# Performance work log

Hardware: AMD Instinct MI355X
Metric: run time of the kernel (lower is better)

Reference implementation:

```python
import jax, jax.numpy as jnp
import numpy as np

L = 104          # atom feature / hidden dim (self.length)
NUM_CLASSES = 500
D, N, P = 256, 1024, 8  # DAGs, nodes per DAG (topo-ordered), max predecessors


def setup_inputs() -> dict:
    key = jax.random.key(0)
    ks = jax.random.split(key, 8)
    atom_features = jax.random.normal(ks[0], (D, N, L), dtype=jnp.float32)

    # Padded predecessor lists; pred_idx[d, n, p] < n guarantees topological order 0..N-1.
    rng = np.random.default_rng(0)
    base = np.floor(rng.random((D, N, P)) * np.maximum(np.arange(N), 1)[None, :, None]).astype(np.int32)
    keep = rng.random((D, N, P)) < 0.6
    keep[:, :, 0] = True                      # every non-root node has >=1 predecessor
    pred_idx = np.where(keep, base, -1)
    pred_idx[:, 0, :] = -1                    # node 0 is the root (no predecessors)
    pred_idx = jnp.asarray(pred_idx, dtype=jnp.int32)

    s1 = float(1.0 / np.sqrt(L))
    s2 = float(1.0 / np.sqrt(2 * L))
    W_single = jax.random.uniform(ks[1], (L, L), minval=-s1, maxval=s1)
    b_single = jax.random.uniform(ks[2], (L,), minval=-s1, maxval=s1)
    W_merge = jax.random.uniform(ks[3], (L, 2 * L), minval=-s2, maxval=s2)
    b_merge = jax.random.uniform(ks[4], (L,), minval=-s2, maxval=s2)
    attn_w = jax.random.uniform(ks[5], (L,))   # torch.rand(length)
    dag_w = jax.random.uniform(ks[6], (L,))
    W_final = jax.random.uniform(ks[7], (NUM_CLASSES, L), minval=-s1, maxval=s1)
    b_final = jnp.zeros((NUM_CLASSES,), jnp.float32)
    return {
        "atom_features": atom_features, "pred_idx": pred_idx,
        "W_single": W_single, "b_single": b_single,
        "W_merge": W_merge, "b_merge": b_merge,
        "attn_w": attn_w, "dag_w": dag_w,
        "W_final": W_final, "b_final": b_final,
    }


def _forward(atom_features, pred_idx, W_single, b_single, W_merge, b_merge,
             attn_w, dag_w, W_final, b_final):
    n_nodes = atom_features.shape[1]

    def per_dag(feats, preds):  # feats [N, L], preds [N, P]
        def step(outputs, n):
            feat = feats[n]                                   # [L]
            p = preds[n]                                      # [P]
            valid = p >= 0                                    # [P]
            po = outputs[jnp.clip(p, 0, n_nodes - 1)]         # [P, L] gathered predecessor outputs
            # softmax over the predecessor (stacking) dim, weighted by attention_weight
            logits = jnp.where(valid[:, None], attn_w * po, -1e30)
            agg = jnp.sum(jax.nn.softmax(logits, axis=0) * po * valid[:, None].astype(po.dtype), axis=0)  # [L]
            merged = jax.nn.relu(W_merge @ jnp.concatenate([agg, feat]) + b_merge)
            root = jax.nn.relu(W_single @ feat + b_single)
            out = jnp.where(jnp.any(valid), merged, root)     # [L]
            return outputs.at[n].set(out), None
        outputs, _ = jax.lax.scan(step, jnp.zeros_like(feats), jnp.arange(n_nodes))
        return outputs[-1]                                    # output of last (sink) node

    last = jax.vmap(per_dag)(atom_features, pred_idx)         # [D, L]
    w = jax.nn.softmax(dag_w * last, axis=0)                  # softmax over DAG dim
    pooled = jnp.sum(w * last, axis=0)                        # [L]
    return pooled @ W_final.T + b_final                       # [NUM_CLASSES]


def reference(atom_features, pred_idx, W_single, b_single, W_merge, b_merge,
              attn_w, dag_w, W_final, b_final):
    return _forward(atom_features, pred_idx, W_single, b_single, W_merge, b_merge,
                    attn_w, dag_w, W_final, b_final)
```

## Files before the change

kernel.cpp:

```cpp
#include <hip/hip_runtime.h>

#define DN  256
#define NN  1024
#define PP  8
#define LL  104
#define CLS 500
#define BT  512
#define TMAX 64
#define KP  232
#define NG  26

typedef __attribute__((ext_vector_type(8))) short short8;
typedef __attribute__((ext_vector_type(4))) short short4v;
typedef __attribute__((ext_vector_type(4))) float f32x4;

#define MFMA(a, b, c) __builtin_amdgcn_mfma_f32_16x16x32_bf16((a), (b), (c), 0, 0, 0)

__device__ __forceinline__ void split_bf16(float x, unsigned short& h, unsigned short& l) {
    unsigned u = __float_as_uint(x);
    h = (unsigned short)(u >> 16);
    float hf = __uint_as_float(u & 0xFFFF0000u);
    l = (unsigned short)(__float_as_uint(x - hf) >> 16);
}

__global__ __launch_bounds__(BT, 2) void dag_level_kernel(
    const float* __restrict__ atom,
    const int*   __restrict__ pred,
    const float* __restrict__ W_single,
    const float* __restrict__ b_single,
    const float* __restrict__ W_merge,
    const float* __restrict__ b_merge,
    const float* __restrict__ attn_w,
    float* __restrict__ out_all,
    float* __restrict__ last_buf)
{
    __shared__ __align__(16) unsigned short x_hi[TMAX][KP];
    __shared__ __align__(16) unsigned short x_lo[TMAX][KP];
    __shared__ int   lvl[NN];
    __shared__ int   cnt[NN];
    __shared__ unsigned short order[NN];
    __shared__ __align__(16) float s_attn2[LL];
    __shared__ float s_bm[LL];
    __shared__ int   csum[64];
    __shared__ int   s_flag, s_maxlvl;

    const int d    = blockIdx.x;
    const int tid  = threadIdx.x;
    const int wid  = tid >> 6;
    const int lane = tid & 63;
    const int p    = wid & 3;

    const float* atom_d = atom + (size_t)d * NN * LL;
    const int*   pred_d = pred + (size_t)d * NN * PP;
    float*       out_d  = out_all + (size_t)d * NN * LL;

    short8 wh[2][7], wl[2][7];
    #pragma unroll
    for (int h = 0; h < 2; ++h) {
        const int r = (2*p + h)*16 + (lane & 15);
        #pragma unroll
        for (int kt = 0; kt < 7; ++kt) {
            const int k0 = kt*32 + (lane >> 4)*8;
            short8 hh, lo8;
            #pragma unroll
            for (int j = 0; j < 8; ++j) {
                float v = (r < LL && (k0 + j) < 2*LL) ? W_merge[r*2*LL + k0 + j] : 0.f;
                unsigned short a, b;
                split_bf16(v, a, b);
                hh[j] = (short)a; lo8[j] = (short)b;
            }
            wh[h][kt] = hh; wl[h][kt] = lo8;
        }
    }

    for (int idx = tid; idx < TMAX * (KP - 2*LL); idx += BT) {
        int rr = idx / (KP - 2*LL), cc = 2*LL + (idx - rr*(KP - 2*LL));
        x_hi[rr][cc] = 0; x_lo[rr][cc] = 0;
    }
    if (tid < LL) { s_attn2[tid] = attn_w[tid] * 1.44269504f; s_bm[tid] = b_merge[tid]; }
    if (tid == 0) { s_flag = 0; s_maxlvl = 0; }

    {
        int mypA[PP], mypB[PP];
        const int4* p4 = (const int4*)(pred_d + tid * PP);
        int4 a = p4[0], b = p4[1];
        mypA[0]=a.x; mypA[1]=a.y; mypA[2]=a.z; mypA[3]=a.w;
        mypA[4]=b.x; mypA[5]=b.y; mypA[6]=b.z; mypA[7]=b.w;
        const int4* q4 = (const int4*)(pred_d + (tid + BT) * PP);
        int4 c = q4[0], e = q4[1];
        mypB[0]=c.x; mypB[1]=c.y; mypB[2]=c.z; mypB[3]=c.w;
        mypB[4]=e.x; mypB[5]=e.y; mypB[6]=e.z; mypB[7]=e.w;
        lvl[tid] = 0; lvl[tid + BT] = 0;
        __syncthreads();
        for (int it = 1; it <= NN; ++it) {
            int mxA = -1, mxB = -1;
            #pragma unroll
            for (int q = 0; q < PP; ++q) {
                if (mypA[q] >= 0) mxA = max(mxA, lvl[mypA[q]]);
                if (mypB[q] >= 0) mxB = max(mxB, lvl[mypB[q]]);
            }
            bool ch = false;
            if (mxA + 1 != lvl[tid])      { lvl[tid]      = mxA + 1; ch = true; }
            if (mxB + 1 != lvl[tid + BT]) { lvl[tid + BT] = mxB + 1; ch = true; }
            if (ch) s_flag = it;
            __syncthreads();
            int f = s_flag;
            __syncthreads();
            if (f != it) break;
        }
        atomicMax(&s_maxlvl, max(lvl[tid], lvl[tid + BT]));
    }

    cnt[tid] = 0; cnt[tid + BT] = 0;
    __syncthreads();
    atomicAdd(&cnt[lvl[tid]], 1);
    atomicAdd(&cnt[lvl[tid + BT]], 1);
    __syncthreads();
    if (tid < 64) { int s = 0; for (int i = 0; i < 16; ++i) s += cnt[tid*16 + i]; csum[tid] = s; }
    __syncthreads();
    if (tid == 0) { int run = 0; for (int t = 0; t < 64; ++t) { int c = csum[t]; csum[t] = run; run += c; } }
    __syncthreads();
    if (tid < 64) {
        int run = csum[tid];
        for (int i = 0; i < 16; ++i) { int c = cnt[tid*16 + i]; cnt[tid*16 + i] = run; run += c; }
    }
    __syncthreads();
    {
        int pos = atomicAdd(&cnt[lvl[tid]], 1);      order[pos] = (unsigned short)tid;
        pos     = atomicAdd(&cnt[lvl[tid + BT]], 1); order[pos] = (unsigned short)(tid + BT);
    }
    __syncthreads();

    {
        int nroots = cnt[0];
        for (int task = tid; task < nroots * LL; task += BT) {
            int ni = task / LL, r = task - ni * LL;
            int n = order[ni];
            float acc = b_single[r];
            const float* feat = atom_d + n * LL;
            const float* wr = W_single + r * LL;
            #pragma unroll 8
            for (int l = 0; l < LL; ++l) acc = fmaf(wr[l], feat[l], acc);
            float v = fmaxf(acc, 0.f);
            out_d[n * LL + r] = v;
            if (n == NN - 1) last_buf[d * LL + r] = v;
        }
    }
    __syncthreads();

    const int maxlvl = s_maxlvl;
    for (int L = 1; L <= maxlvl; ++L) {
        const int s = cnt[L - 1], e = cnt[L];
        for (int t0 = s; t0 < e; t0 += TMAX) {
            const int tc = min(TMAX, e - t0);

            const int ntask = tc * NG;
            for (int task = tid; task < ntask; task += BT) {
                int ni = task / NG;
                int lg = task - ni * NG;
                int n  = order[t0 + ni];
                const int4* pp4 = (const int4*)(pred_d + n * PP);
                int4 pa = pp4[0], pb = pp4[1];
                int pi[PP] = {pa.x, pa.y, pa.z, pa.w, pb.x, pb.y, pb.z, pb.w};
                float4 po4[PP];
                #pragma unroll
                for (int q = 0; q < PP; ++q) {
                    int idx = max(pi[q], 0);
                    po4[q] = *(const float4*)&out_d[idx * LL + lg * 4];
                }
                float4 ft = *(const float4*)&atom_d[n * LL + lg * 4];
                float4 aw = *(const float4*)&s_attn2[lg * 4];
                float po[PP][4];
                #pragma unroll
                for (int q = 0; q < PP; ++q) {
                    po[q][0] = po4[q].x; po[q][1] = po4[q].y;
                    po[q][2] = po4[q].z; po[q][3] = po4[q].w;
                }
                float awv[4] = {aw.x, aw.y, aw.z, aw.w};
                float ftv[4] = {ft.x, ft.y, ft.z, ft.w};
                unsigned short oh[8], ol[8];
                #pragma unroll
                for (int f = 0; f < 4; ++f) {
                    float den = 0.f, num = 0.f;
                    #pragma unroll
                    for (int q = 0; q < PP; ++q) {
                        float e2 = exp2f(awv[f] * po[q][f]);
                        e2 = (pi[q] >= 0) ? e2 : 0.f;
                        den += e2;
                        num = fmaf(e2, po[q][f], num);
                    }
                    float agg = __fdividef(num, den);
                    split_bf16(agg,    oh[f],     ol[f]);
                    split_bf16(ftv[f], oh[4 + f], ol[4 + f]);
                }
                short4v h0 = {(short)oh[0], (short)oh[1], (short)oh[2], (short)oh[3]};
                short4v l0 = {(short)ol[0], (short)ol[1], (short)ol[2], (short)ol[3]};
                short4v h1 = {(short)oh[4], (short)oh[5], (short)oh[6], (short)oh[7]};
                short4v l1 = {(short)ol[4], (short)ol[5], (short)ol[6], (short)ol[7]};
                *(short4v*)&x_hi[ni][lg*4]      = h0;
                *(short4v*)&x_lo[ni][lg*4]      = l0;
                *(short4v*)&x_hi[ni][LL + lg*4] = h1;
                *(short4v*)&x_lo[ni][LL + lg*4] = l1;
            }
            __syncthreads();

            const int mts = (tc + 15) >> 4;
            const int njobs = mts * 4;
            for (int job = wid; job < njobs; job += 8) {
                const int mt = job >> 2;
                const int row_a = mt*16 + (lane & 15);
                const int kg = (lane >> 4) * 8;
                f32x4 a0 = {0.f,0.f,0.f,0.f}, b0 = {0.f,0.f,0.f,0.f}, c0 = {0.f,0.f,0.f,0.f};
                f32x4 a1 = {0.f,0.f,0.f,0.f}, b1 = {0.f,0.f,0.f,0.f}, c1 = {0.f,0.f,0.f,0.f};
                #pragma unroll
                for (int kt = 0; kt < 7; ++kt) {
                    const int k0 = kt*32 + kg;
                    short8 ah = *(const short8*)&x_hi[row_a][k0];
                    short8 al = *(const short8*)&x_lo[row_a][k0];
                    a0 = MFMA(ah, wh[0][kt], a0);
                    b0 = MFMA(ah, wl[0][kt], b0);
                    c0 = MFMA(al, wh[0][kt], c0);
                    if (p < 3) {
                        a1 = MFMA(ah, wh[1][kt], a1);
                        b1 = MFMA(ah, wl[1][kt], b1);
                        c1 = MFMA(al, wh[1][kt], c1);
                    }
                }
                f32x4 acc0 = a0 + b0 + c0;
                f32x4 acc1 = a1 + b1 + c1;
                const int r0 = p*32 + (lane & 15);
                #pragma unroll
                for (int j = 0; j < 4; ++j) {
                    int ni = mt*16 + (lane >> 4)*4 + j;
                    if (ni < tc) {
                        int n = order[t0 + ni];
                        if (r0 < LL) {
                            float v = fmaxf(acc0[j] + s_bm[r0], 0.f);
                            out_d[n*LL + r0] = v;
                            if (n == NN - 1) last_buf[d*LL + r0] = v;
                        }
                        if (p < 3) {
                            const int r1 = r0 + 16;
                            float v = fmaxf(acc1[j] + s_bm[r1], 0.f);
                            out_d[n*LL + r1] = v;
                            if (n == NN - 1) last_buf[d*LL + r1] = v;
                        }
                    }
                }
            }
            __syncthreads();
        }
    }
}

__global__ __launch_bounds__(256) void final_pool_kernel(
    const float* __restrict__ last_buf,
    const float* __restrict__ dag_w,
    const float* __restrict__ W_final,
    const float* __restrict__ b_final,
    float* __restrict__ out)
{
    __shared__ float s_pooled[LL];
    const int tid = threadIdx.x;

    if (tid < LL) {
        float dw = dag_w[tid];
        float m = -1e30f;
        #pragma unroll 8
        for (int dd = 0; dd < DN; ++dd)
            m = fmaxf(m, dw * last_buf[dd * LL + tid]);
        float den = 0.f, num = 0.f;
        #pragma unroll 8
        for (int dd = 0; dd < DN; ++dd) {
            float v = last_buf[dd * LL + tid];
            float e = __expf(dw * v - m);
            den += e;
            num = fmaf(e, v, num);
        }
        s_pooled[tid] = num / den;
    }
    __syncthreads();

    for (int c = tid; c < CLS; c += 256) {
        float acc = b_final[c];
        const float* wr = W_final + c * LL;
        #pragma unroll 8
        for (int l = 0; l < LL; ++l) acc = fmaf(wr[l], s_pooled[l], acc);
        out[c] = acc;
    }
}

extern "C" void kernel_launch(void* const* d_in, const int* in_sizes, int n_in,
                              void* d_out, int out_size, void* d_ws, size_t ws_size,
                              hipStream_t stream) {
    const float* atom     = (const float*)d_in[0];
    const int*   pred     = (const int*)  d_in[1];
    const float* W_single = (const float*)d_in[2];
    const float* b_single = (const float*)d_in[3];
    const float* W_merge  = (const float*)d_in[4];
    const float* b_merge  = (const float*)d_in[5];
    const float* attn_w   = (const float*)d_in[6];
    const float* dag_w    = (const float*)d_in[7];
    const float* W_final  = (const float*)d_in[8];
    const float* b_final  = (const float*)d_in[9];
    float* out = (float*)d_out;

    float* out_all  = (float*)d_ws;
    float* last_buf = out_all + (size_t)DN * NN * LL;

    dag_level_kernel<<<DN, BT, 0, stream>>>(atom, pred, W_single, b_single,
                                            W_merge, b_merge, attn_w,
                                            out_all, last_buf);
    final_pool_kernel<<<1, 256, 0, stream>>>(last_buf, dag_w, W_final, b_final, out);
}
```

Measured before the change: 367.5 us.

## Software-pipeline predecessor gathers and assign one output tile per wave

The aggregation loop is software-pipelined with two register stages, so the global gathers for the next task are issued before the softmax math of the current one, hiding memory latency. The MFMA stage changes from four waves each holding two 16-row weight tiles to seven waves each holding one tile and looping over all node tiles. This halves the per-wave weight registers and spreads the matmul over more waves, but it leaves one wave idle and doubles the live gather registers. The duplicated loads clamp the task index to stay in range.

```diff
diff --git a/kernel.cpp b/kernel.cpp
--- a/kernel.cpp
+++ b/kernel.cpp
@@ -48,16 +48,14 @@
     const int tid  = threadIdx.x;
     const int wid  = tid >> 6;
     const int lane = tid & 63;
-    const int p    = wid & 3;
 
     const float* atom_d = atom + (size_t)d * NN * LL;
     const int*   pred_d = pred + (size_t)d * NN * PP;
     float*       out_d  = out_all + (size_t)d * NN * LL;
 
-    short8 wh[2][7], wl[2][7];
-    #pragma unroll
-    for (int h = 0; h < 2; ++h) {
-        const int r = (2*p + h)*16 + (lane & 15);
+    short8 wh[7], wl[7];
+    {
+        const int r = min(wid, 6)*16 + (lane & 15);
         #pragma unroll
         for (int kt = 0; kt < 7; ++kt) {
             const int k0 = kt*32 + (lane >> 4)*8;
@@ -69,7 +67,7 @@
                 split_bf16(v, a, b);
                 hh[j] = (short)a; lo8[j] = (short)b;
             }
-            wh[h][kt] = hh; wl[h][kt] = lo8;
+            wh[kt] = hh; wl[kt] = lo8;
         }
     }
 
@@ -148,102 +146,102 @@
     }
     __syncthreads();
 
+#define DECLP(S) int pi##S[PP]; float4 po##S[PP]; float4 ft##S; int ni##S, lg##S;
+
+#define LOADP(S, TASK)                                                          \
+    {                                                                           \
+        int tt_ = min((TASK), ntask - 1);                                       \
+        ni##S = tt_ / NG; lg##S = tt_ - ni##S * NG;                             \
+        int n_ = order[t0 + ni##S];                                             \
+        const int4* pp4_ = (const int4*)(pred_d + n_ * PP);                     \
+        int4 pa_ = pp4_[0], pb_ = pp4_[1];                                      \
+        pi##S[0]=pa_.x; pi##S[1]=pa_.y; pi##S[2]=pa_.z; pi##S[3]=pa_.w;         \
+        pi##S[4]=pb_.x; pi##S[5]=pb_.y; pi##S[6]=pb_.z; pi##S[7]=pb_.w;         \
+        ft##S = *(const float4*)&atom_d[n_ * LL + lg##S * 4];                   \
+        _Pragma("unroll")                                                       \
+        for (int q_ = 0; q_ < PP; ++q_) {                                       \
+            int idx_ = max(pi##S[q_], 0);                                       \
+            po##S[q_] = *(const float4*)&out_d[idx_ * LL + lg##S * 4];          \
+        }                                                                       \
+    }
+
+#define COMPP(S)                                                                \
+    {                                                                           \
+        float4 aw_ = *(const float4*)&s_attn2[lg##S * 4];                       \
+        float awv_[4] = {aw_.x, aw_.y, aw_.z, aw_.w};                           \
+        float ftv_[4] = {ft##S.x, ft##S.y, ft##S.z, ft##S.w};                   \
+        unsigned short oh_[8], ol_[8];                                          \
+        _Pragma("unroll")                                                       \
+        for (int f_ = 0; f_ < 4; ++f_) {                                        \
+            float den_ = 0.f, num_ = 0.f;                                       \
+            _Pragma("unroll")                                                   \
+            for (int q_ = 0; q_ < PP; ++q_) {                                   \
+                float pv_ = ((const float*)&po##S[q_])[f_];                     \
+                float e_ = exp2f(awv_[f_] * pv_);                               \
+                e_ = (pi##S[q_] >= 0) ? e_ : 0.f;                               \
+                den_ += e_;                                                     \
+                num_ = fmaf(e_, pv_, num_);                                     \
+            }                                                                   \
+            float agg_ = __fdividef(num_, den_);                                \
+            split_bf16(agg_,      oh_[f_],     ol_[f_]);                        \
+            split_bf16(ftv_[f_],  oh_[4+f_],   ol_[4+f_]);                      \
+        }                                                                       \
+        short4v h0_ = {(short)oh_[0], (short)oh_[1], (short)oh_[2], (short)oh_[3]}; \
+        short4v l0_ = {(short)ol_[0], (short)ol_[1], (short)ol_[2], (short)ol_[3]}; \
+        short4v h1_ = {(short)oh_[4], (short)oh_[5], (short)oh_[6], (short)oh_[7]}; \
+        short4v l1_ = {(short)ol_[4], (short)ol_[5], (short)ol_[6], (short)ol_[7]}; \
+        *(short4v*)&x_hi[ni##S][lg##S*4]      = h0_;                            \
+        *(short4v*)&x_lo[ni##S][lg##S*4]      = l0_;                            \
+        *(short4v*)&x_hi[ni##S][LL + lg##S*4] = h1_;                            \
+        *(short4v*)&x_lo[ni##S][LL + lg##S*4] = l1_;                            \
+    }
+
     const int maxlvl = s_maxlvl;
     for (int L = 1; L <= maxlvl; ++L) {
         const int s = cnt[L - 1], e = cnt[L];
         for (int t0 = s; t0 < e; t0 += TMAX) {
             const int tc = min(TMAX, e - t0);
-
             const int ntask = tc * NG;
-            for (int task = tid; task < ntask; task += BT) {
-                int ni = task / NG;
-                int lg = task - ni * NG;
-                int n  = order[t0 + ni];
-                const int4* pp4 = (const int4*)(pred_d + n * PP);
-                int4 pa = pp4[0], pb = pp4[1];
-                int pi[PP] = {pa.x, pa.y, pa.z, pa.w, pb.x, pb.y, pb.z, pb.w};
-                float4 po4[PP];
-                #pragma unroll
-                for (int q = 0; q < PP; ++q) {
-                    int idx = max(pi[q], 0);
-                    po4[q] = *(const float4*)&out_d[idx * LL + lg * 4];
+
+            {
+                DECLP(A) DECLP(B)
+                LOADP(A, tid)
+                for (int t = tid; t < ntask; t += 2*BT) {
+                    LOADP(B, t + BT)
+                    COMPP(A)
+                    if (t + 2*BT < ntask) LOADP(A, t + 2*BT)
+                    COMPP(B)
                 }
-                float4 ft = *(const float4*)&atom_d[n * LL + lg * 4];
-                float4 aw = *(const float4*)&s_attn2[lg * 4];
-                float po[PP][4];
-                #pragma unroll
-                for (int q = 0; q < PP; ++q) {
-                    po[q][0] = po4[q].x; po[q][1] = po4[q].y;
-                    po[q][2] = po4[q].z; po[q][3] = po4[q].w;
-                }
-                float awv[4] = {aw.x, aw.y, aw.z, aw.w};
-                float ftv[4] = {ft.x, ft.y, ft.z, ft.w};
-                unsigned short oh[8], ol[8];
-                #pragma unroll
-                for (int f = 0; f < 4; ++f) {
-                    float den = 0.f, num = 0.f;
-                    #pragma unroll
-                    for (int q = 0; q < PP; ++q) {
-                        float e2 = exp2f(awv[f] * po[q][f]);
-                        e2 = (pi[q] >= 0) ? e2 : 0.f;
-                        den += e2;
-                        num = fmaf(e2, po[q][f], num);
-                    }
-                    float agg = __fdividef(num, den);
-                    split_bf16(agg,    oh[f],     ol[f]);
-                    split_bf16(ftv[f], oh[4 + f], ol[4 + f]);
-                }
-                short4v h0 = {(short)oh[0], (short)oh[1], (short)oh[2], (short)oh[3]};
-                short4v l0 = {(short)ol[0], (short)ol[1], (short)ol[2], (short)ol[3]};
-                short4v h1 = {(short)oh[4], (short)oh[5], (short)oh[6], (short)oh[7]};
-                short4v l1 = {(short)ol[4], (short)ol[5], (short)ol[6], (short)ol[7]};
-                *(short4v*)&x_hi[ni][lg*4]      = h0;
-                *(short4v*)&x_lo[ni][lg*4]      = l0;
-                *(short4v*)&x_hi[ni][LL + lg*4] = h1;
-                *(short4v*)&x_lo[ni][LL + lg*4] = l1;
             }
             __syncthreads();
 
-            const int mts = (tc + 15) >> 4;
-            const int njobs = mts * 4;
-            for (int job = wid; job < njobs; job += 8) {
-                const int mt = job >> 2;
-                const int row_a = mt*16 + (lane & 15);
+            if (wid < 7) {
+                const int mts = (tc + 15) >> 4;
                 const int kg = (lane >> 4) * 8;
-                f32x4 a0 = {0.f,0.f,0.f,0.f}, b0 = {0.f,0.f,0.f,0.f}, c0 = {0.f,0.f,0.f,0.f};
-                f32x4 a1 = {0.f,0.f,0.f,0.f}, b1 = {0.f,0.f,0.f,0.f}, c1 = {0.f,0.f,0.f,0.f};
-                #pragma unroll
-                for (int kt = 0; kt < 7; ++kt) {
-                    const int k0 = kt*32 + kg;
-                    short8 ah = *(const short8*)&x_hi[row_a][k0];
-                    short8 al = *(const short8*)&x_lo[row_a][k0];
-                    a0 = MFMA(ah, wh[0][kt], a0);
-                    b0 = MFMA(ah, wl[0][kt], b0);
-                    c0 = MFMA(al, wh[0][kt], c0);
-                    if (p < 3) {
-                        a1 = MFMA(ah, wh[1][kt], a1);
-                        b1 = MFMA(ah, wl[1][kt], b1);
-                        c1 = MFMA(al, wh[1][kt], c1);
+                const int r0 = wid*16 + (lane & 15);
+                for (int mt = 0; mt < mts; ++mt) {
+                    const int row_a = mt*16 + (lane & 15);
+                    f32x4 a0 = {0.f,0.f,0.f,0.f}, b0 = {0.f,0.f,0.f,0.f}, c0 = {0.f,0.f,0.f,0.f};
+                    #pragma unroll
+                    for (int kt = 0; kt < 7; ++kt) {
+                        const int k0 = kt*32 + kg;
+                        short8 ah = *(const short8*)&x_hi[row_a][k0];
+                        short8 al = *(const short8*)&x_lo[row_a][k0];
+                        a0 = MFMA(ah, wh[kt], a0);
+                        b0 = MFMA(ah, wl[kt], b0);
+                        c0 = MFMA(al, wh[kt], c0);
                     }
-                }
-                f32x4 acc0 = a0 + b0 + c0;
-                f32x4 acc1 = a1 + b1 + c1;
-                const int r0 = p*32 + (lane & 15);
-                #pragma unroll
-                for (int j = 0; j < 4; ++j) {
-                    int ni = mt*16 + (lane >> 4)*4 + j;
-                    if (ni < tc) {
-                        int n = order[t0 + ni];
-                        if (r0 < LL) {
-                            float v = fmaxf(acc0[j] + s_bm[r0], 0.f);
-                            out_d[n*LL + r0] = v;
-                            if (n == NN - 1) last_buf[d*LL + r0] = v;
-                        }
-                        if (p < 3) {
-                            const int r1 = r0 + 16;
-                            float v = fmaxf(acc1[j] + s_bm[r1], 0.f);
-                            out_d[n*LL + r1] = v;
-                            if (n == NN - 1) last_buf[d*LL + r1] = v;
+                    f32x4 acc = a0 + b0 + c0;
+                    if (r0 < LL) {
+                        #pragma unroll
+                        for (int j = 0; j < 4; ++j) {
+                            int ni = mt*16 + (lane >> 4)*4 + j;
+                            if (ni < tc) {
+                                int n = order[t0 + ni];
+                                float v = fmaxf(acc[j] + s_bm[r0], 0.f);
+                                out_d[n*LL + r0] = v;
+                                if (n == NN - 1) last_buf[d*LL + r0] = v;
+                            }
                         }
                     }
                 }
@@ -251,6 +249,9 @@
             __syncthreads();
         }
     }
+#undef DECLP
+#undef LOADP
+#undef COMPP
 }
 
 __global__ __launch_bounds__(256) void final_pool_kernel(
```

After: 401.1 us. 1.09x slower.

## Prefetch next level's gathers during MFMA and stage predecessor lists in LDS

Applied to the files above, without the earlier changes.

Copies the predecessor index table into LDS once and uses it for level computation and gathers. Before the merge GEMM of the current tile, it issues the next tile's feature loads and predecessor-output loads, reloading only predecessors that sit at the level being computed now. It also doubles the relaxation steps per barrier in level assignment and remaps the MFMA work so seven waves each own one 16-row slice of the weights. The aim is to hide global-memory latency behind the MFMA phase and reduce barriers, at the cost of more registers and 32KB more LDS, which may reduce occupancy.

```diff
diff --git a/kernel.cpp b/kernel.cpp
--- a/kernel.cpp
+++ b/kernel.cpp
@@ -21,6 +21,39 @@
     h = (unsigned short)(u >> 16);
     float hf = __uint_as_float(u & 0xFFFF0000u);
     l = (unsigned short)(__float_as_uint(x - hf) >> 16);
+}
+
+__device__ __forceinline__ void sm_store(int ni, int lg, const int pi[PP],
+    const float4 pv[PP], float4 ft, const float* s_attn2,
+    unsigned short (*xh)[KP], unsigned short (*xl)[KP])
+{
+    float4 aw = *(const float4*)&s_attn2[lg * 4];
+    float awv[4] = {aw.x, aw.y, aw.z, aw.w};
+    float ftv[4] = {ft.x, ft.y, ft.z, ft.w};
+    unsigned short oh[8], ol[8];
+    #pragma unroll
+    for (int f = 0; f < 4; ++f) {
+        float den = 0.f, num = 0.f;
+        #pragma unroll
+        for (int q = 0; q < PP; ++q) {
+            float pvq = ((const float*)&pv[q])[f];
+            float e2 = exp2f(awv[f] * pvq);
+            e2 = (pi[q] >= 0) ? e2 : 0.f;
+            den += e2;
+            num = fmaf(e2, pvq, num);
+        }
+        float agg = __fdividef(num, den);
+        split_bf16(agg,    oh[f],     ol[f]);
+        split_bf16(ftv[f], oh[4 + f], ol[4 + f]);
+    }
+    short4v h0 = {(short)oh[0], (short)oh[1], (short)oh[2], (short)oh[3]};
+    short4v l0 = {(short)ol[0], (short)ol[1], (short)ol[2], (short)ol[3]};
+    short4v h1 = {(short)oh[4], (short)oh[5], (short)oh[6], (short)oh[7]};
+    short4v l1 = {(short)ol[4], (short)ol[5], (short)ol[6], (short)ol[7]};
+    *(short4v*)&xh[ni][lg*4]      = h0;
+    *(short4v*)&xl[ni][lg*4]      = l0;
+    *(short4v*)&xh[ni][LL + lg*4] = h1;
+    *(short4v*)&xl[ni][LL + lg*4] = l1;
 }
 
 __global__ __launch_bounds__(BT, 2) void dag_level_kernel(
@@ -36,6 +69,7 @@
 {
     __shared__ __align__(16) unsigned short x_hi[TMAX][KP];
     __shared__ __align__(16) unsigned short x_lo[TMAX][KP];
+    __shared__ __align__(16) int pred_lds[NN][PP];
     __shared__ int   lvl[NN];
     __shared__ int   cnt[NN];
     __shared__ unsigned short order[NN];
@@ -48,16 +82,17 @@
     const int tid  = threadIdx.x;
     const int wid  = tid >> 6;
     const int lane = tid & 63;
-    const int p    = wid & 3;
 
     const float* atom_d = atom + (size_t)d * NN * LL;
     const int*   pred_d = pred + (size_t)d * NN * PP;
     float*       out_d  = out_all + (size_t)d * NN * LL;
 
-    short8 wh[2][7], wl[2][7];
-    #pragma unroll
-    for (int h = 0; h < 2; ++h) {
-        const int r = (2*p + h)*16 + (lane & 15);
+    for (int idx = tid; idx < NN * PP / 4; idx += BT)
+        ((int4*)pred_lds)[idx] = ((const int4*)pred_d)[idx];
+
+    short8 wh[7], wl[7];
+    {
+        const int r = min(wid, 6)*16 + (lane & 15);
         #pragma unroll
         for (int kt = 0; kt < 7; ++kt) {
             const int k0 = kt*32 + (lane >> 4)*8;
@@ -69,7 +104,7 @@
                 split_bf16(v, a, b);
                 hh[j] = (short)a; lo8[j] = (short)b;
             }
-            wh[h][kt] = hh; wl[h][kt] = lo8;
+            wh[kt] = hh; wl[kt] = lo8;
         }
     }
 
@@ -79,29 +114,26 @@
     }
     if (tid < LL) { s_attn2[tid] = attn_w[tid] * 1.44269504f; s_bm[tid] = b_merge[tid]; }
     if (tid == 0) { s_flag = 0; s_maxlvl = 0; }
+    lvl[tid] = 0; lvl[tid + BT] = 0;
+    __syncthreads();
 
     {
         int mypA[PP], mypB[PP];
-        const int4* p4 = (const int4*)(pred_d + tid * PP);
-        int4 a = p4[0], b = p4[1];
-        mypA[0]=a.x; mypA[1]=a.y; mypA[2]=a.z; mypA[3]=a.w;
-        mypA[4]=b.x; mypA[5]=b.y; mypA[6]=b.z; mypA[7]=b.w;
-        const int4* q4 = (const int4*)(pred_d + (tid + BT) * PP);
-        int4 c = q4[0], e = q4[1];
-        mypB[0]=c.x; mypB[1]=c.y; mypB[2]=c.z; mypB[3]=c.w;
-        mypB[4]=e.x; mypB[5]=e.y; mypB[6]=e.z; mypB[7]=e.w;
-        lvl[tid] = 0; lvl[tid + BT] = 0;
-        __syncthreads();
+        #pragma unroll
+        for (int q = 0; q < PP; ++q) { mypA[q] = pred_lds[tid][q]; mypB[q] = pred_lds[tid + BT][q]; }
         for (int it = 1; it <= NN; ++it) {
-            int mxA = -1, mxB = -1;
+            bool ch = false;
             #pragma unroll
-            for (int q = 0; q < PP; ++q) {
-                if (mypA[q] >= 0) mxA = max(mxA, lvl[mypA[q]]);
-                if (mypB[q] >= 0) mxB = max(mxB, lvl[mypB[q]]);
-            }
-            bool ch = false;
-            if (mxA + 1 != lvl[tid])      { lvl[tid]      = mxA + 1; ch = true; }
-            if (mxB + 1 != lvl[tid + BT]) { lvl[tid + BT] = mxB + 1; ch = true; }
+            for (int rep = 0; rep < 2; ++rep) {
+                int mxA = -1, mxB = -1;
+                #pragma unroll
+                for (int q = 0; q < PP; ++q) {
+                    if (mypA[q] >= 0) mxA = max(mxA, lvl[mypA[q]]);
+                    if (mypB[q] >= 0) mxB = max(mxB, lvl[mypB[q]]);
+                }
+                if (mxA + 1 != lvl[tid])      { lvl[tid]      = mxA + 1; ch = true; }
+                if (mxB + 1 != lvl[tid + BT]) { lvl[tid + BT] = mxB + 1; ch = true; }
+            }
             if (ch) s_flag = it;
             __syncthreads();
             int f = s_flag;
@@ -149,101 +181,109 @@
     __syncthreads();
 
     const int maxlvl = s_maxlvl;
+
+    float4 pf_po[PP];
+    float4 pf_ft = {0.f, 0.f, 0.f, 0.f};
+    int    pf_fresh = 0;
+
+#define PREFETCH(NT0, NTC, LCUR) do {                                          \
+        pf_fresh = 0;                                                          \
+        if (tid < (NTC) * NG) {                                                \
+            int ni_ = tid / NG, lg_ = tid - ni_ * NG;                          \
+            int n_ = order[(NT0) + ni_];                                       \
+            pf_ft = *(const float4*)&atom_d[n_ * LL + lg_ * 4];                \
+            _Pragma("unroll")                                                  \
+            for (int q_ = 0; q_ < PP; ++q_) {                                  \
+                int pi_ = pred_lds[n_][q_];                                    \
+                bool fr_ = (pi_ >= 0) && (lvl[pi_] == (LCUR));                 \
+                int row_ = fr_ ? 0 : max(pi_, 0);                              \
+                pf_fresh |= (fr_ ? 1 : 0) << q_;                               \
+                pf_po[q_] = *(const float4*)&out_d[row_ * LL + lg_ * 4];       \
+            }                                                                  \
+        }                                                                      \
+    } while (0)
+
+    if (maxlvl >= 1) {
+        int s1 = cnt[0];
+        int ntc0 = min(TMAX, cnt[1] - s1);
+        PREFETCH(s1, ntc0, 0);
+    }
+
     for (int L = 1; L <= maxlvl; ++L) {
         const int s = cnt[L - 1], e = cnt[L];
         for (int t0 = s; t0 < e; t0 += TMAX) {
             const int tc = min(TMAX, e - t0);
-
             const int ntask = tc * NG;
-            for (int task = tid; task < ntask; task += BT) {
-                int ni = task / NG;
-                int lg = task - ni * NG;
-                int n  = order[t0 + ni];
-                const int4* pp4 = (const int4*)(pred_d + n * PP);
-                int4 pa = pp4[0], pb = pp4[1];
-                int pi[PP] = {pa.x, pa.y, pa.z, pa.w, pb.x, pb.y, pb.z, pb.w};
-                float4 po4[PP];
+
+            if (tid < ntask) {
+                int ni = tid / NG, lg = tid - ni * NG;
+                int n = order[t0 + ni];
+                int pi[PP];
+                #pragma unroll
+                for (int q = 0; q < PP; ++q) pi[q] = pred_lds[n][q];
+                float4 rg[PP];
                 #pragma unroll
                 for (int q = 0; q < PP; ++q) {
-                    int idx = max(pi[q], 0);
-                    po4[q] = *(const float4*)&out_d[idx * LL + lg * 4];
+                    int row = ((pf_fresh >> q) & 1) ? pi[q] : 0;
+                    rg[q] = *(const float4*)&out_d[row * LL + lg * 4];
+                }
+                float4 pv[PP];
+                #pragma unroll
+                for (int q = 0; q < PP; ++q)
+                    pv[q] = ((pf_fresh >> q) & 1) ? rg[q] : pf_po[q];
+                sm_store(ni, lg, pi, pv, pf_ft, s_attn2, x_hi, x_lo);
+            }
+            for (int task = tid + BT; task < ntask; task += BT) {
+                int ni = task / NG, lg = task - ni * NG;
+                int n = order[t0 + ni];
+                int pi[PP];
+                #pragma unroll
+                for (int q = 0; q < PP; ++q) pi[q] = pred_lds[n][q];
+                float4 pv[PP];
+                #pragma unroll
+                for (int q = 0; q < PP; ++q) {
+                    int row = max(pi[q], 0);
+                    pv[q] = *(const float4*)&out_d[row * LL + lg * 4];
                 }
                 float4 ft = *(const float4*)&atom_d[n * LL + lg * 4];
-                float4 aw = *(const float4*)&s_attn2[lg * 4];
-                float po[PP][4];
-                #pragma unroll
-                for (int q = 0; q < PP; ++q) {
-                    po[q][0] = po4[q].x; po[q][1] = po4[q].y;
-                    po[q][2] = po4[q].z; po[q][3] = po4[q].w;
-                }
-                float awv[4] = {aw.x, aw.y, aw.z, aw.w};
-                float ftv[4] = {ft.x, ft.y, ft.z, ft.w};
-                unsigned short oh[8], ol[8];
-                #pragma unroll
-                for (int f = 0; f < 4; ++f) {
-                    float den = 0.f, num = 0.f;
+                sm_store(ni, lg, pi, pv, ft, s_attn2, x_hi, x_lo);
+            }
+            __syncthreads();
+
+            {
+                int nt0 = 0, ntc = 0;
+                if (t0 + TMAX < e)        { nt0 = t0 + TMAX; ntc = min(TMAX, e - nt0); }
+                else if (L + 1 <= maxlvl) { nt0 = e;         ntc = min(TMAX, cnt[L + 1] - e); }
+                PREFETCH(nt0, ntc, L);
+            }
+
+            if (wid < 7) {
+                const int mts = (tc + 15) >> 4;
+                const int kg = (lane >> 4) * 8;
+                const int r0 = wid*16 + (lane & 15);
+                for (int mt = 0; mt < mts; ++mt) {
+                    const int row_a = mt*16 + (lane & 15);
+                    f32x4 a0 = {0.f,0.f,0.f,0.f}, b0 = {0.f,0.f,0.f,0.f}, c0 = {0.f,0.f,0.f,0.f};
                     #pragma unroll
-                    for (int q = 0; q < PP; ++q) {
-                        float e2 = exp2f(awv[f] * po[q][f]);
-                        e2 = (pi[q] >= 0) ? e2 : 0.f;
-                        den += e2;
-                        num = fmaf(e2, po[q][f], num);
+                    for (int kt = 0; kt < 7; ++kt) {
+                        const int k0 = kt*32 + kg;
+                        short8 ah = *(const short8*)&x_hi[row_a][k0];
+                        short8 al = *(const short8*)&x_lo[row_a][k0];
+                        a0 = MFMA(ah, wh[kt], a0);
+                        b0 = MFMA(ah, wl[kt], b0);
+                        c0 = MFMA(al, wh[kt], c0);
                     }
-                    float agg = __fdividef(num, den);
-                    split_bf16(agg,    oh[f],     ol[f]);
-                    split_bf16(ftv[f], oh[4 + f], ol[4 + f]);
-                }
-                short4v h0 = {(short)oh[0], (short)oh[1], (short)oh[2], (short)oh[3]};
-                short4v l0 = {(short)ol[0], (short)ol[1], (short)ol[2], (short)ol[3]};
-                short4v h1 = {(short)oh[4], (short)oh[5], (short)oh[6], (short)oh[7]};
-                short4v l1 = {(short)ol[4], (short)ol[5], (short)ol[6], (short)ol[7]};
-                *(short4v*)&x_hi[ni][lg*4]      = h0;
-                *(short4v*)&x_lo[ni][lg*4]      = l0;
-                *(short4v*)&x_hi[ni][LL + lg*4] = h1;
-                *(short4v*)&x_lo[ni][LL + lg*4] = l1;
-            }
-            __syncthreads();
-
-            const int mts = (tc + 15) >> 4;
-            const int njobs = mts * 4;
-            for (int job = wid; job < njobs; job += 8) {
-                const int mt = job >> 2;
-                const int row_a = mt*16 + (lane & 15);
-                const int kg = (lane >> 4) * 8;
-                f32x4 a0 = {0.f,0.f,0.f,0.f}, b0 = {0.f,0.f,0.f,0.f}, c0 = {0.f,0.f,0.f,0.f};
-                f32x4 a1 = {0.f,0.f,0.f,0.f}, b1 = {0.f,0.f,0.f,0.f}, c1 = {0.f,0.f,0.f,0.f};
-                #pragma unroll
-                for (int kt = 0; kt < 7; ++kt) {
-                    const int k0 = kt*32 + kg;
-                    short8 ah = *(const short8*)&x_hi[row_a][k0];
-                    short8 al = *(const short8*)&x_lo[row_a][k0];
-                    a0 = MFMA(ah, wh[0][kt], a0);
-                    b0 = MFMA(ah, wl[0][kt], b0);
-                    c0 = MFMA(al, wh[0][kt], c0);
-                    if (p < 3) {
-                        a1 = MFMA(ah, wh[1][kt], a1);
-                        b1 = MFMA(ah, wl[1][kt], b1);
-                        c1 = MFMA(al, wh[1][kt], c1);
-                    }
-                }
-                f32x4 acc0 = a0 + b0 + c0;
-                f32x4 acc1 = a1 + b1 + c1;
-                const int r0 = p*32 + (lane & 15);
-                #pragma unroll
-                for (int j = 0; j < 4; ++j) {
-                    int ni = mt*16 + (lane >> 4)*4 + j;
-                    if (ni < tc) {
-                        int n = order[t0 + ni];
-                        if (r0 < LL) {
-                            float v = fmaxf(acc0[j] + s_bm[r0], 0.f);
-                            out_d[n*LL + r0] = v;
-                            if (n == NN - 1) last_buf[d*LL + r0] = v;
-                        }
-                        if (p < 3) {
-                            const int r1 = r0 + 16;
-                            float v = fmaxf(acc1[j] + s_bm[r1], 0.f);
-                            out_d[n*LL + r1] = v;
-                            if (n == NN - 1) last_buf[d*LL + r1] = v;
+                    f32x4 acc = a0 + b0 + c0;
+                    if (r0 < LL) {
+                        #pragma unroll
+                        for (int j = 0; j < 4; ++j) {
+                            int ni = mt*16 + (lane >> 4)*4 + j;
+                            if (ni < tc) {
+                                int n = order[t0 + ni];
+                                float v = fmaxf(acc[j] + s_bm[r0], 0.f);
+                                out_d[n*LL + r0] = v;
+                                if (n == NN - 1) last_buf[d*LL + r0] = v;
+                            }
                         }
                     }
                 }
@@ -251,6 +291,7 @@
             __syncthreads();
         }
     }
+#undef PREFETCH
 }
 
 __global__ __launch_bounds__(256) void final_pool_kernel(
```

Result: slower. 387.8 us (+5.5%).
